# Optimization experiments

Hardware: AMD Instinct MI355X
Metric: run time of the kernel (lower is better)

The kernel has to match this reference:

```python
import jax, jax.numpy as jnp
import numpy as np
from functools import partial

D = 512      # world_state_dim
M = 1000     # memory_size
H = 8        # attention heads
DH = D // H  # head dim
EPS = 1e-5


def _layernorm(x, g, b):
    mu = jnp.mean(x, axis=-1, keepdims=True)
    var = jnp.mean((x - mu) ** 2, axis=-1, keepdims=True)
    return (x - mu) * jax.lax.rsqrt(var + EPS) * g + b


def setup_inputs() -> dict:
    key = jax.random.key(0)
    ks = jax.random.split(key, 24)
    B = 8192
    w = lambda k, shp: (jax.random.normal(k, shp, dtype=jnp.float32) * 0.02)
    inp = {
        "observations": jax.random.normal(ks[0], (B, D), dtype=jnp.float32),
        "ego_motion": jax.random.normal(ks[1], (B, 16), dtype=jnp.float32),
        "world_memory": jax.random.normal(ks[2], (M, D), dtype=jnp.float32) * 0.1,
        # encoder: Linear(D,D) -> ReLU -> LN(D) -> Linear(D,D)
        "enc_w1": w(ks[3], (D, D)), "enc_b1": jnp.zeros((D,), jnp.float32),
        "enc_g": jnp.ones((D,), jnp.float32), "enc_beta": jnp.zeros((D,), jnp.float32),
        "enc_w2": w(ks[4], (D, D)), "enc_b2": jnp.zeros((D,), jnp.float32),
        # multihead attention in/out projections
        "wq": w(ks[5], (D, D)), "bq": jnp.zeros((D,), jnp.float32),
        "wk": w(ks[6], (D, D)), "bk": jnp.zeros((D,), jnp.float32),
        "wv": w(ks[7], (D, D)), "bv": jnp.zeros((D,), jnp.float32),
        "wo": w(ks[8], (D, D)), "bo": jnp.zeros((D,), jnp.float32),
        # transition: Linear(D+16,D) -> ReLU -> LN(D) -> Linear(D,D)
        "tr_w1": w(ks[9], (D, D + 16)), "tr_b1": jnp.zeros((D,), jnp.float32),
        "tr_g": jnp.ones((D,), jnp.float32), "tr_beta": jnp.zeros((D,), jnp.float32),
        "tr_w2": w(ks[10], (D, D)), "tr_b2": jnp.zeros((D,), jnp.float32),
        # quality head: Linear(D,128) -> ReLU -> Linear(128,1) -> Sigmoid
        "q_w1": w(ks[11], (128, D)), "q_b1": jnp.zeros((128,), jnp.float32),
        "q_w2": w(ks[12], (1, 128)), "q_b2": jnp.zeros((1,), jnp.float32),
        # random slots for memory-bank scatter-EMA update (replaces torch.randint)
        "update_indices": jax.random.randint(ks[13], (B,), 0, M, dtype=jnp.int32),
    }
    return inp


def _forward_core(observations, ego_motion, world_memory,
                  enc_w1, enc_b1, enc_g, enc_beta, enc_w2, enc_b2,
                  wq, bq, wk, bk, wv, bv, wo, bo,
                  tr_w1, tr_b1, tr_g, tr_beta, tr_w2, tr_b2,
                  q_w1, q_b1, q_w2, q_b2):
    B = observations.shape[0]
    # world_encoder
    h = jax.nn.relu(observations @ enc_w1.T + enc_b1)
    encoded = _layernorm(h, enc_g, enc_beta) @ enc_w2.T + enc_b2  # [B, D]
    # cross-attention: one query per batch row over shared memory bank
    q = (encoded @ wq.T + bq).reshape(B, H, DH)
    k = (world_memory @ wk.T + bk).reshape(M, H, DH)  # shared across batch
    v = (world_memory @ wv.T + bv).reshape(M, H, DH)
    scores = jnp.einsum("bhd,mhd->bhm", q, k) / jnp.sqrt(jnp.float32(DH))
    attn = jax.nn.softmax(scores, axis=-1)              # [B, H, M]
    ctx = jnp.einsum("bhm,mhd->bhd", attn, v).reshape(B, D)
    memory_states = ctx @ wo.T + bo
    # fuse + transition
    fused = 0.7 * encoded + 0.3 * memory_states
    x = jnp.concatenate([fused, ego_motion], axis=-1)   # [B, D+16]
    h2 = jax.nn.relu(x @ tr_w1.T + tr_b1)
    next_state = _layernorm(h2, tr_g, tr_beta) @ tr_w2.T + tr_b2  # [B, D]
    # quality head
    qh = jax.nn.relu(next_state @ q_w1.T + q_b1)
    quality = jax.nn.sigmoid(qh @ q_w2.T + q_b2)        # [B, 1]
    mem_weights = jnp.mean(attn, axis=1)                # [B, M] avg over heads
    return next_state, quality, mem_weights


def _update_memory_bank(world_memory, next_state, quality, update_indices):
    # Sequential scatter-EMA, faithful to the torch loop (duplicates compound).
    mask = quality[:, 0] > 0.7

    def step(mem, inp):
        idx, st, m = inp
        row = mem[idx]
        new_row = jnp.where(m, 0.9 * row + 0.1 * st, row)
        return mem.at[idx].set(new_row), None

    updated, _ = jax.lax.scan(step, world_memory, (update_indices, next_state, mask))
    return updated


@jax.jit
def reference(observations, ego_motion, world_memory,
              enc_w1, enc_b1, enc_g, enc_beta, enc_w2, enc_b2,
              wq, bq, wk, bk, wv, bv, wo, bo,
              tr_w1, tr_b1, tr_g, tr_beta, tr_w2, tr_b2,
              q_w1, q_b1, q_w2, q_b2, update_indices):
    next_state, quality, mem_weights = _forward_core(
        observations, ego_motion, world_memory,
        enc_w1, enc_b1, enc_g, enc_beta, enc_w2, enc_b2,
        wq, bq, wk, bk, wv, bv, wo, bo,
        tr_w1, tr_b1, tr_g, tr_beta, tr_w2, tr_b2,
        q_w1, q_b1, q_w2, q_b2)
    updated_memory = _update_memory_bank(world_memory, next_state, quality, update_indices)
    return next_state, quality, updated_memory
```

## Files before the change

kernel.cpp:

```cpp
#include <hip/hip_runtime.h>

#define B_ 8192
#define D_ 512
#define M_ 1000
#define H_ 8
#define LOG2E 1.4426950408889634f

typedef unsigned short u16;
typedef __attribute__((ext_vector_type(8))) short bf16x8;
typedef __attribute__((ext_vector_type(4))) float f32x4;

__device__ __forceinline__ float bf2f(u16 u) {
    union { unsigned u; float f; } c; c.u = ((unsigned)u) << 16; return c.f;
}
__device__ __forceinline__ u16 f2bf(float f) {
    union { float f; unsigned u; } c; c.f = f;
    unsigned r = (c.u + 0x7fffu + ((c.u >> 16) & 1u)) >> 16;
    return (u16)r;
}
__device__ __forceinline__ u16 f2bf_fast(float f) {
    union { float f; unsigned u; } c; c.f = f;
    return (u16)((c.u + 0x8000u) >> 16);
}
__device__ __forceinline__ float wave_sum(float v) {
#pragma unroll
    for (int off = 32; off > 0; off >>= 1) v += __shfl_xor(v, off);
    return v;
}

template<bool RELU, bool WF32, bool VTOUT>
__device__ __forceinline__ void gemm_core(
    const u16* __restrict__ A0, const u16* __restrict__ A1,
    const u16* __restrict__ A2, int lda0, int lda1, int lda2,
    const u16* __restrict__ W0, const u16* __restrict__ W1,
    const u16* __restrict__ W2, int ldw0, int ldw1, int ldw2,
    int kb1, int kb2,
    const float* __restrict__ bias, float bscale, float cscale,
    float* __restrict__ Cf, u16* __restrict__ Cb, u16* __restrict__ VT,
    int M, int N, int K, int ldc)
{
    const int m0 = blockIdx.y * 64, n0 = blockIdx.x * 64;
    if (m0 >= M || n0 >= N) return;
    __shared__ u16 As[64 * 64];
    __shared__ u16 Bs[64 * 64];
    const int t = threadIdx.x, w = t >> 6, l = t & 63;
    const int wm = (w >> 1) * 32, wn = (w & 1) * 32;
    const int li = l & 15, quad = l >> 4;

    f32x4 acc[2][2];
#pragma unroll
    for (int i = 0; i < 2; ++i)
#pragma unroll
        for (int j = 0; j < 2; ++j) acc[i][j] = (f32x4){0.f, 0.f, 0.f, 0.f};

    for (int k0 = 0; k0 < K; k0 += 64) {
        const u16* Ab; const u16* Wb; int ldab, ldwb, ko;
        if (k0 < kb1)      { Ab = A0; ldab = lda0; Wb = W0; ldwb = ldw0; ko = k0; }
        else if (k0 < kb2) { Ab = A1; ldab = lda1; Wb = W1; ldwb = ldw1; ko = k0 - kb1; }
        else               { Ab = A2; ldab = lda2; Wb = W2; ldwb = ldw2; ko = k0 - kb2; }
#pragma unroll
        for (int i = 0; i < 2; ++i) {
            const int rl = w * 16 + i * 8 + (l >> 3);
            const int ck = (l & 7) ^ (rl & 7);
            int ga = m0 + rl; ga = ga < M ? ga : M - 1;
            __builtin_amdgcn_global_load_lds(
                (const __attribute__((address_space(1))) void*)(Ab + (size_t)ga * ldab + ko + ck * 8),
                (__attribute__((address_space(3))) void*)(As + (w * 16 + i * 8) * 64),
                16, 0, 0);
        }
#pragma unroll
        for (int i = 0; i < 2; ++i) {
            const int rl = w * 16 + i * 8 + (l >> 3);
            const int ck = (l & 7) ^ (rl & 7);
            int gb = n0 + rl; gb = gb < N ? gb : N - 1;
            __builtin_amdgcn_global_load_lds(
                (const __attribute__((address_space(1))) void*)(Wb + (size_t)gb * ldwb + ko + ck * 8),
                (__attribute__((address_space(3))) void*)(Bs + (w * 16 + i * 8) * 64),
                16, 0, 0);
        }
        __syncthreads();
#pragma unroll
        for (int ks = 0; ks < 2; ++ks) {
            const int ch = ks * 4 + quad;
            bf16x8 af[2], bfr[2];
#pragma unroll
            for (int mt = 0; mt < 2; ++mt) {
                const int r = wm + mt * 16 + li;
                af[mt] = *(const bf16x8*)(As + r * 64 + ((ch ^ (r & 7)) * 8));
            }
#pragma unroll
            for (int nt = 0; nt < 2; ++nt) {
                const int r = wn + nt * 16 + li;
                bfr[nt] = *(const bf16x8*)(Bs + r * 64 + ((ch ^ (r & 7)) * 8));
            }
#pragma unroll
            for (int mt = 0; mt < 2; ++mt)
#pragma unroll
                for (int nt = 0; nt < 2; ++nt)
                    acc[mt][nt] = __builtin_amdgcn_mfma_f32_16x16x32_bf16(
                        af[mt], bfr[nt], acc[mt][nt], 0, 0, 0);
        }
        __syncthreads();
    }

    float bv[2];
#pragma unroll
    for (int nt = 0; nt < 2; ++nt) bv[nt] = bias[n0 + wn + nt * 16 + li] * bscale;
#pragma unroll
    for (int mt = 0; mt < 2; ++mt) {
        const int row0 = m0 + wm + mt * 16 + quad * 4;
#pragma unroll
        for (int nt = 0; nt < 2; ++nt) {
            const int col = n0 + wn + nt * 16 + li;
            if (VTOUT && col >= 512) {
                ushort4 pk;
                u16 pv[4];
#pragma unroll
                for (int r = 0; r < 4; ++r) {
                    float v = acc[mt][nt][r] * cscale + bv[nt];
                    pv[r] = (row0 + r < M_) ? f2bf(v) : (u16)0;
                }
                pk.x = pv[0]; pk.y = pv[1]; pk.z = pv[2]; pk.w = pv[3];
                *(ushort4*)(VT + (size_t)(col - 512) * 1024 + row0) = pk;
            } else {
#pragma unroll
                for (int r = 0; r < 4; ++r) {
                    const int row = row0 + r;
                    if (row >= M) continue;
                    float v = acc[mt][nt][r] * cscale + bv[nt];
                    if (RELU) v = fmaxf(v, 0.f);
                    Cb[(size_t)row * ldc + col] = f2bf(v);
                    if (WF32) Cf[(size_t)row * ldc + col] = v;
                }
            }
        }
    }
}

template<bool RELU, bool WF32>
__launch_bounds__(256)
__global__ void mgemm(const u16* __restrict__ A0, const u16* __restrict__ A1,
                      const u16* __restrict__ A2, int lda0, int lda1, int lda2,
                      const u16* __restrict__ W0, const u16* __restrict__ W1,
                      const u16* __restrict__ W2, int ldw0, int ldw1, int ldw2,
                      int kb1, int kb2,
                      const float* __restrict__ bias, float bscale, float cscale,
                      float* __restrict__ Cf, u16* __restrict__ Cb,
                      int M, int N, int K, int ldc)
{
    gemm_core<RELU, WF32, false>(A0, A1, A2, lda0, lda1, lda2,
                                 W0, W1, W2, ldw0, ldw1, ldw2, kb1, kb2,
                                 bias, bscale, cscale, Cf, Cb, nullptr, M, N, K, ldc);
}

__launch_bounds__(256)
__global__ void foldgemm(const u16* __restrict__ w_q, const u16* __restrict__ w_tr1,
                         const u16* __restrict__ w_e2t, const u16* __restrict__ w_wot,
                         const float* __restrict__ zb,
                         u16* __restrict__ w_qe, u16* __restrict__ w_ae,
                         u16* __restrict__ w_co)
{
    const int z = blockIdx.z;
    if (z == 0)
        gemm_core<false, false, false>(w_q, w_q, w_q, 512, 512, 512,
            w_e2t, w_e2t, w_e2t, 512, 512, 512, 512, 512,
            zb, 0.f, 1.0f, nullptr, w_qe, nullptr, 512, 512, 512, 512);
    else if (z == 1)
        gemm_core<false, false, false>(w_tr1, w_tr1, w_tr1, 576, 576, 576,
            w_e2t, w_e2t, w_e2t, 512, 512, 512, 512, 512,
            zb, 0.f, 0.7f, nullptr, w_ae, nullptr, 512, 512, 512, 512);
    else
        gemm_core<false, false, false>(w_tr1, w_tr1, w_tr1, 576, 576, 576,
            w_wot, w_wot, w_wot, 512, 512, 512, 512, 512,
            zb, 0.f, 0.3f, nullptr, w_co, nullptr, 512, 512, 512, 512);
}

__launch_bounds__(256)
__global__ void qkvgemm(const u16* __restrict__ hn, const u16* __restrict__ w_qe,
                        const float* __restrict__ bqe, u16* __restrict__ qbuf,
                        const u16* __restrict__ wmem_bf, const u16* __restrict__ w_k,
                        const float* __restrict__ bkv, u16* __restrict__ KVbuf,
                        u16* __restrict__ VTb)
{
    if (blockIdx.z == 0)
        gemm_core<false, false, false>(hn, hn, hn, 512, 512, 512,
            w_qe, w_qe, w_qe, 512, 512, 512, 512, 512,
            bqe, 1.f, 1.f, nullptr, qbuf, nullptr, B_, 512, 512, 512);
    else
        gemm_core<false, false, true>(wmem_bf, wmem_bf, wmem_bf, 512, 512, 512,
            w_k, w_k, w_k, 512, 512, 512, 512, 512,
            bkv, 1.f, 1.f, nullptr, KVbuf, VTb, 1024, 1024, 512, 1024);
}

__launch_bounds__(256)
__global__ void attn_kernel(const u16* __restrict__ Q, const u16* __restrict__ KV,
                            const u16* __restrict__ VT, u16* __restrict__ Ob,
                            float* __restrict__ Lb)
{
    __shared__ u16 P[4 * 2048];
    const int t = threadIdx.x, w = t >> 6, l = t & 63;
    const int h = blockIdx.y;
    const int qblk = blockIdx.x & 63, kpart = blockIdx.x >> 6;
    const int q0 = qblk * 128 + w * 32;
    u16* Pw = P + w * 2048;
    const int li = l & 15, quad = l >> 4;

    bf16x8 aq[2][2];
#pragma unroll
    for (int mt = 0; mt < 2; ++mt)
#pragma unroll
        for (int ks = 0; ks < 2; ++ks) {
            const int row = q0 + mt * 16 + li;
            aq[mt][ks] = *(const bf16x8*)(Q + (size_t)row * 512 + h * 64 + ks * 32 + quad * 8);
        }

    bf16x8 ones;
#pragma unroll
    for (int i = 0; i < 8; ++i) ones[i] = (short)0x3F80;

    f32x4 oacc[2][4];
    f32x4 lacc[2];
#pragma unroll
    for (int mt = 0; mt < 2; ++mt) {
        lacc[mt] = (f32x4){0.f, 0.f, 0.f, 0.f};
#pragma unroll
        for (int nt = 0; nt < 4; ++nt) oacc[mt][nt] = (f32x4){0.f, 0.f, 0.f, 0.f};
    }

    const int kbeg = kpart * 512, kend = kbeg + 512;
    for (int kc = kbeg; kc < kend; kc += 64) {
        f32x4 s[2][4];
#pragma unroll
        for (int mt = 0; mt < 2; ++mt)
#pragma unroll
            for (int nt = 0; nt < 4; ++nt) s[mt][nt] = (f32x4){0.f, 0.f, 0.f, 0.f};
#pragma unroll
        for (int ks = 0; ks < 2; ++ks) {
            bf16x8 bk[4];
#pragma unroll
            for (int nt = 0; nt < 4; ++nt) {
                const int key = kc + nt * 16 + li;
                bk[nt] = *(const bf16x8*)(KV + (size_t)key * 1024 + h * 64 + ks * 32 + quad * 8);
            }
#pragma unroll
            for (int mt = 0; mt < 2; ++mt)
#pragma unroll
                for (int nt = 0; nt < 4; ++nt)
                    s[mt][nt] = __builtin_amdgcn_mfma_f32_16x16x32_bf16(
                        aq[mt][ks], bk[nt], s[mt][nt], 0, 0, 0);
        }
        if (kc == 960) {
#pragma unroll
            for (int nt = 0; nt < 4; ++nt) {
                const bool val = (960 + nt * 16 + li) < M_;
#pragma unroll
                for (int mt = 0; mt < 2; ++mt)
#pragma unroll
                    for (int r = 0; r < 4; ++r)
                        if (!val) s[mt][nt][r] = -3.0e38f;
            }
        }
#pragma unroll
        for (int mt = 0; mt < 2; ++mt)
#pragma unroll
            for (int nt = 0; nt < 4; ++nt) {
                const int col = nt * 16 + li;
#pragma unroll
                for (int r = 0; r < 4; ++r) {
                    const float p = exp2f(s[mt][nt][r]);
                    const int rowl = mt * 16 + quad * 4 + r;
                    Pw[rowl * 64 + (((col >> 3) ^ (rowl & 7)) * 8) + (col & 7)] = f2bf_fast(p);
                }
            }
#pragma unroll
        for (int ks = 0; ks < 2; ++ks) {
            const int ch = ks * 4 + quad;
            bf16x8 ap[2];
#pragma unroll
            for (int mt = 0; mt < 2; ++mt) {
                const int rowl = mt * 16 + li;
                ap[mt] = *(const bf16x8*)(Pw + rowl * 64 + ((ch ^ (rowl & 7)) * 8));
            }
#pragma unroll
            for (int mt = 0; mt < 2; ++mt)
                lacc[mt] = __builtin_amdgcn_mfma_f32_16x16x32_bf16(
                    ap[mt], ones, lacc[mt], 0, 0, 0);
#pragma unroll
            for (int nt = 0; nt < 4; ++nt) {
                const bf16x8 bvv = *(const bf16x8*)(VT + ((size_t)(h * 64 + nt * 16 + li)) * 1024 + kc + ks * 32 + quad * 8);
#pragma unroll
                for (int mt = 0; mt < 2; ++mt)
                    oacc[mt][nt] = __builtin_amdgcn_mfma_f32_16x16x32_bf16(
                        ap[mt], bvv, oacc[mt][nt], 0, 0, 0);
            }
        }
    }

    u16* Op = Ob + (size_t)kpart * B_ * 512;
    float* Lp = Lb + (size_t)kpart * B_ * 8;
#pragma unroll
    for (int mt = 0; mt < 2; ++mt)
#pragma unroll
        for (int r = 0; r < 4; ++r) {
            const int row = q0 + mt * 16 + quad * 4 + r;
            if (li == 0) Lp[row * 8 + h] = lacc[mt][r];
#pragma unroll
            for (int nt = 0; nt < 4; ++nt)
                Op[(size_t)row * 512 + h * 64 + nt * 16 + li] = f2bf(oacc[mt][nt][r]);
        }
}

__launch_bounds__(256)
__global__ void attn_combine(const u16* __restrict__ Ob, const float* __restrict__ Lb,
                             u16* __restrict__ ctx)
{
    const int row = blockIdx.x * 4 + (threadIdx.x >> 6);
    const int lane = threadIdx.x & 63;
    const int h = lane >> 3;
    const float inv = 1.0f / (Lb[row * 8 + h] + Lb[(size_t)B_ * 8 + row * 8 + h]);
    const u16* p0 = Ob + (size_t)row * 512 + lane * 8;
    const u16* p1 = p0 + (size_t)B_ * 512;
    uint4 a = *(const uint4*)p0;
    uint4 b = *(const uint4*)p1;
    const unsigned aa[4] = {a.x, a.y, a.z, a.w};
    const unsigned bb[4] = {b.x, b.y, b.z, b.w};
    unsigned o[4];
#pragma unroll
    for (int i = 0; i < 4; ++i) {
        const float lo = (bf2f((u16)(aa[i] & 0xffffu)) + bf2f((u16)(bb[i] & 0xffffu))) * inv;
        const float hi = (bf2f((u16)(aa[i] >> 16)) + bf2f((u16)(bb[i] >> 16))) * inv;
        o[i] = (unsigned)f2bf(lo) | ((unsigned)f2bf(hi) << 16);
    }
    *(uint4*)(ctx + (size_t)row * 512 + lane * 8) = make_uint4(o[0], o[1], o[2], o[3]);
}

__launch_bounds__(256)
__global__ void ln_bf(u16* __restrict__ X, const float* __restrict__ g,
                      const float* __restrict__ be, int rows)
{
    const int row = blockIdx.x * 4 + (threadIdx.x >> 6);
    const int lane = threadIdx.x & 63;
    if (row >= rows) return;
    u16* p = X + (size_t)row * 512 + lane * 8;
    uint4 d = *(const uint4*)p;
    const unsigned dd[4] = {d.x, d.y, d.z, d.w};
    float v[8];
#pragma unroll
    for (int i = 0; i < 4; ++i) {
        v[2 * i]     = bf2f((u16)(dd[i] & 0xffffu));
        v[2 * i + 1] = bf2f((u16)(dd[i] >> 16));
    }
    float s = 0.f;
#pragma unroll
    for (int i = 0; i < 8; ++i) s += v[i];
    s = wave_sum(s);
    const float mu = s * (1.0f / 512.0f);
    float vs = 0.f;
#pragma unroll
    for (int i = 0; i < 8; ++i) { v[i] -= mu; vs += v[i] * v[i]; }
    vs = wave_sum(vs);
    const float r = rsqrtf(vs * (1.0f / 512.0f) + 1e-5f);
    const float* gp = g + lane * 8;
    const float* bp = be + lane * 8;
    unsigned o[4];
#pragma unroll
    for (int i = 0; i < 4; ++i) {
        const u16 lo = f2bf(v[2 * i] * r * gp[2 * i] + bp[2 * i]);
        const u16 hi = f2bf(v[2 * i + 1] * r * gp[2 * i + 1] + bp[2 * i + 1]);
        o[i] = (unsigned)lo | ((unsigned)hi << 16);
    }
    *(uint4*)p = make_uint4(o[0], o[1], o[2], o[3]);
}

__launch_bounds__(256)
__global__ void prep_all(const float* enc_w1, const float* wk_f, const float* wv_f,
                         const float* tr_w2, const float* q_w1, const float* wq,
                         const float* tr_w1, const float* enc_w2, const float* wo,
                         const float* obs, const float* wmem, const float* ego,
                         const float* bk, const float* bvv, const float* bq,
                         const float* enc_b2, const float* trb1, const float* bo,
                         u16* w_enc1, u16* w_k, u16* w_v, u16* w_tr2, u16* w_qh,
                         u16* w_q, u16* w_tr1, u16* w_e2t, u16* w_wot,
                         u16* obs_bf, u16* wmem_bf, u16* ego64,
                         float* bkv, float* bqe, float* btr)
{
    __shared__ float tl[64][65];
    const int seg = blockIdx.y;
    const int t = threadIdx.x;
    const int bx = blockIdx.x;

    if (seg <= 5) {
        const float* s; u16* d; int n; float sc = 1.0f;
        switch (seg) {
            case 0: s = enc_w1; d = w_enc1; n = 262144; break;
            case 1: s = wk_f;   d = w_k;    n = 262144; break;
            case 2: s = wv_f;   d = w_v;    n = 262144; break;
            case 3: s = tr_w2;  d = w_tr2;  n = 262144; break;
            case 4: s = q_w1;   d = w_qh;   n = 65536;  break;
            default: s = wq;    d = w_q;    n = 262144; sc = 0.125f * LOG2E; break;
        }
        const int i0 = (bx * 256 + t) * 4;
        if (i0 + 3 < n) {
            const float4 v = *(const float4*)(s + i0);
            ushort4 o;
            o.x = f2bf(v.x * sc); o.y = f2bf(v.y * sc);
            o.z = f2bf(v.z * sc); o.w = f2bf(v.w * sc);
            *(ushort4*)(d + i0) = o;
        }
    } else if (seg == 6) {
#pragma unroll
        for (int k = 0; k < 4; ++k) {
            const int i = (bx * 256 + t) * 4 + k;
            if (i < 294912) {
                const int r = i / 576, c = i - r * 576;
                w_tr1[i] = (c < 528) ? f2bf(tr_w1[r * 528 + c]) : (u16)0;
            }
        }
    } else if (seg <= 8) {
        if (bx >= 64) return;
        const float* S = (seg == 7) ? enc_w2 : wo;
        u16* D = (seg == 7) ? w_e2t : w_wot;
        const int r0 = (bx >> 3) * 64, c0 = (bx & 7) * 64;
#pragma unroll
        for (int i = 0; i < 16; ++i) {
            const int idx = t + i * 256;
            tl[idx >> 6][idx & 63] = S[(size_t)(r0 + (idx >> 6)) * 512 + c0 + (idx & 63)];
        }
        __syncthreads();
#pragma unroll
        for (int i = 0; i < 16; ++i) {
            const int idx = t + i * 256;
            const int c = idx >> 6, r = idx & 63;
            D[(size_t)(c0 + c) * 512 + r0 + r] = f2bf(tl[r][c]);
        }
    } else if (seg == 9) {
        const int nth = gridDim.x * 256;
        for (int i = bx * 256 + t; i < B_ * 512 / 4; i += nth) {
            const float4 v = ((const float4*)obs)[i];
            ushort4 o;
            o.x = f2bf(v.x); o.y = f2bf(v.y); o.z = f2bf(v.z); o.w = f2bf(v.w);
            ((ushort4*)obs_bf)[i] = o;
        }
    } else if (seg == 10) {
        const int nth = gridDim.x * 256;
        for (int i = bx * 256 + t; i < M_ * 512 / 4; i += nth) {
            const float4 v = ((const float4*)wmem)[i];
            ushort4 o;
            o.x = f2bf(v.x); o.y = f2bf(v.y); o.z = f2bf(v.z); o.w = f2bf(v.w);
            ((ushort4*)wmem_bf)[i] = o;
        }
    } else if (seg == 11) {
        const int nth = gridDim.x * 256;
        for (int i = bx * 256 + t; i < B_ * 64; i += nth) {
            const int b = i >> 6, j = i & 63;
            ego64[(size_t)b * 64 + j] = (j < 16) ? f2bf(ego[b * 16 + j]) : (u16)0;
        }
        const int tid = bx * 256 + t;
        if (tid < 1024) bkv[tid] = (tid < 512) ? bk[tid] : bvv[tid - 512];
    } else {
        if (bx >= 128) return;
        const int i = bx * 4 + (t >> 6);
        const int lane = t & 63;
        float s = 0.f;
        if (seg == 12) {
            const float* wr = wq + (size_t)i * 512 + lane * 8;
#pragma unroll
            for (int j = 0; j < 8; ++j) s += wr[j] * enc_b2[lane * 8 + j];
            s = wave_sum(s);
            if (lane == 0) bqe[i] = 0.125f * LOG2E * (bq[i] + s);
        } else {
            const float* wr = tr_w1 + (size_t)i * 528 + lane * 8;
#pragma unroll
            for (int j = 0; j < 8; ++j)
                s += wr[j] * (0.7f * enc_b2[lane * 8 + j] + 0.3f * bo[lane * 8 + j]);
            s = wave_sum(s);
            if (lane == 0) btr[i] = trb1[i] + s;
        }
    }
}

__global__ void quality_bf(const u16* __restrict__ qh, const float* __restrict__ w2,
                           const float* __restrict__ b2, float* __restrict__ outq,
                           int rows)
{
    const int row = blockIdx.x * 4 + (threadIdx.x >> 6);
    const int lane = threadIdx.x & 63;
    if (row >= rows) return;
    const u16* p = qh + (size_t)row * 128;
    float s = bf2f(p[lane]) * w2[lane] + bf2f(p[64 + lane]) * w2[64 + lane];
    s = wave_sum(s);
    if (lane == 0) outq[row] = 1.0f / (1.0f + expf(-(s + b2[0])));
}

__global__ void compact_kernel(const float* __restrict__ q,
                               int* __restrict__ list, int* __restrict__ cnt)
{
    __shared__ int wtot[16];
    __shared__ int sbase;
    const int t = threadIdx.x, w = t >> 6, lane = t & 63;
    if (t == 0) sbase = 0;
    __syncthreads();
    for (int c = 0; c < B_; c += 1024) {
        const int idx = c + t;
        const bool pred = (q[idx] > 0.7f);
        const unsigned long long bal = __ballot(pred);
        const int prefix = __popcll(bal & ((1ull << lane) - 1ull));
        if (lane == 0) wtot[w] = __popcll(bal);
        __syncthreads();
        int woff = 0;
        for (int i = 0; i < w; ++i) woff += wtot[i];
        if (pred) list[sbase + woff + prefix] = idx;
        __syncthreads();
        if (t == 0) {
            int tot = 0;
            for (int i = 0; i < 16; ++i) tot += wtot[i];
            sbase += tot;
        }
        __syncthreads();
    }
    if (t == 0) *cnt = sbase;
}

__global__ void update_memory_kernel(const float* __restrict__ mem,
                                     const float* __restrict__ ns,
                                     const int* __restrict__ upd,
                                     const int* __restrict__ list,
                                     const int* __restrict__ cnt,
                                     float* __restrict__ outmem)
{
    const int m = blockIdx.x;
    const int t = threadIdx.x;
    const int c4 = t * 4;
    float4 r = *(const float4*)(mem + (size_t)m * D_ + c4);
    const int n = *cnt;
    for (int i = 0; i < n; ++i) {
        const int b = list[i];
        if (upd[b] == m) {
            const float4 s = *(const float4*)(ns + (size_t)b * D_ + c4);
            r.x = 0.9f * r.x + 0.1f * s.x;
            r.y = 0.9f * r.y + 0.1f * s.y;
            r.z = 0.9f * r.z + 0.1f * s.z;
            r.w = 0.9f * r.w + 0.1f * s.w;
        }
    }
    *(float4*)(outmem + (size_t)m * D_ + c4) = r;
}

extern "C" void kernel_launch(void* const* d_in, const int* in_sizes, int n_in,
                              void* d_out, int out_size, void* d_ws, size_t ws_size,
                              hipStream_t stream)
{
    const float* obs    = (const float*)d_in[0];
    const float* ego    = (const float*)d_in[1];
    const float* wmem   = (const float*)d_in[2];
    const float* enc_w1 = (const float*)d_in[3];
    const float* enc_b1 = (const float*)d_in[4];
    const float* enc_g  = (const float*)d_in[5];
    const float* enc_be = (const float*)d_in[6];
    const float* enc_w2 = (const float*)d_in[7];
    const float* enc_b2 = (const float*)d_in[8];
    const float* wq = (const float*)d_in[9];
    const float* bq = (const float*)d_in[10];
    const float* wk_f = (const float*)d_in[11];
    const float* bk = (const float*)d_in[12];
    const float* wv_f = (const float*)d_in[13];
    const float* bvv = (const float*)d_in[14];
    const float* wo = (const float*)d_in[15];
    const float* bo = (const float*)d_in[16];
    const float* tr_w1 = (const float*)d_in[17];
    const float* tr_b1 = (const float*)d_in[18];
    const float* tr_g  = (const float*)d_in[19];
    const float* tr_be = (const float*)d_in[20];
    const float* tr_w2 = (const float*)d_in[21];
    const float* tr_b2 = (const float*)d_in[22];
    const float* q_w1 = (const float*)d_in[23];
    const float* q_b1 = (const float*)d_in[24];
    const float* q_w2 = (const float*)d_in[25];
    const float* q_b2 = (const float*)d_in[26];
    const int*   upd  = (const int*)d_in[27];

    float* out_ns  = (float*)d_out;
    float* out_q   = out_ns + (size_t)B_ * D_;
    float* out_mem = out_q + B_;

    u16* ws = (u16*)d_ws;
    size_t o = 0;
    u16* obs_bf  = ws + o; o += (size_t)B_ * 512;
    u16* wmem_bf = ws + o; o += (size_t)M_ * 512;
    u16* w_enc1  = ws + o; o += 262144;
    u16* w_k     = ws + o; o += 262144;
    u16* w_v     = ws + o; o += 262144;
    u16* w_tr2   = ws + o; o += 262144;
    u16* w_qh    = ws + o; o += 65536;
    u16* w_q     = ws + o; o += 262144;
    u16* w_tr1   = ws + o; o += (size_t)512 * 576;
    u16* w_e2t   = ws + o; o += 262144;
    u16* w_wot   = ws + o; o += 262144;
    u16* w_qe    = ws + o; o += 262144;
    u16* w_ae    = ws + o; o += 262144;
    u16* w_co    = ws + o; o += 262144;
    u16* hbuf    = ws + o; o += (size_t)B_ * 512;
    u16* qbuf    = ws + o; o += (size_t)B_ * 512;
    u16* KVbuf   = ws + o; o += (size_t)1024 * 1024;
    u16* VTb     = ws + o; o += (size_t)512 * 1024;
    u16* ctx     = ws + o; o += (size_t)B_ * 512;
    u16* h2b     = ws + o; o += (size_t)B_ * 512;
    u16* nsbf    = ws + o; o += (size_t)B_ * 512;
    u16* qhb     = ws + o; o += (size_t)B_ * 128;
    u16* ego64   = ws + o; o += (size_t)B_ * 64;
    u16* Obuf    = ws + o; o += (size_t)2 * B_ * 512;
    float* Lbuf  = (float*)(ws + o); o += (size_t)2 * B_ * 8 * 2;
    float* bkv   = (float*)(ws + o); o += 2048;
    float* bqe   = (float*)(ws + o); o += 1024;
    float* btr   = (float*)(ws + o); o += 1024;
    int* list    = (int*)(ws + o);
    int* cnt     = list + B_;

    const dim3 blk(256);

    prep_all<<<dim3(576, 14), blk, 0, stream>>>(
        enc_w1, wk_f, wv_f, tr_w2, q_w1, wq, tr_w1, enc_w2, wo,
        obs, wmem, ego, bk, bvv, bq, enc_b2, tr_b1, bo,
        w_enc1, w_k, w_v, w_tr2, w_qh, w_q, w_tr1, w_e2t, w_wot,
        obs_bf, wmem_bf, ego64, bkv, bqe, btr);

    foldgemm<<<dim3(8, 8, 3), blk, 0, stream>>>(w_q, w_tr1, w_e2t, w_wot, bkv,
                                                w_qe, w_ae, w_co);

    mgemm<true, false><<<dim3(8, 128), blk, 0, stream>>>(
        obs_bf, obs_bf, obs_bf, 512, 512, 512, w_enc1, w_enc1, w_enc1, 512, 512, 512,
        512, 512, enc_b1, 1.f, 1.f, nullptr, hbuf, B_, 512, 512, 512);
    ln_bf<<<dim3(2048), blk, 0, stream>>>(hbuf, enc_g, enc_be, B_);

    qkvgemm<<<dim3(16, 128, 2), blk, 0, stream>>>(
        hbuf, w_qe, bqe, qbuf, wmem_bf, w_k, bkv, KVbuf, VTb);

    attn_kernel<<<dim3(128, 8), blk, 0, stream>>>(qbuf, KVbuf, VTb, Obuf, Lbuf);
    attn_combine<<<dim3(2048), blk, 0, stream>>>(Obuf, Lbuf, ctx);

    mgemm<true, false><<<dim3(8, 128), blk, 0, stream>>>(
        hbuf, ctx, ego64, 512, 512, 64, w_ae, w_co, w_tr1 + 512, 512, 512, 576,
        512, 1024, btr, 1.f, 1.f, nullptr, h2b, B_, 512, 1088, 512);
    ln_bf<<<dim3(2048), blk, 0, stream>>>(h2b, tr_g, tr_be, B_);

    mgemm<false, true><<<dim3(8, 128), blk, 0, stream>>>(
        h2b, h2b, h2b, 512, 512, 512, w_tr2, w_tr2, w_tr2, 512, 512, 512,
        512, 512, tr_b2, 1.f, 1.f, out_ns, nsbf, B_, 512, 512, 512);

    mgemm<true, false><<<dim3(2, 128), blk, 0, stream>>>(
        nsbf, nsbf, nsbf, 512, 512, 512, w_qh, w_qh, w_qh, 512, 512, 512,
        512, 512, q_b1, 1.f, 1.f, nullptr, qhb, B_, 128, 512, 128);
    quality_bf<<<dim3(2048), blk, 0, stream>>>(qhb, q_w2, q_b2, out_q, B_);

    compact_kernel<<<dim3(1), dim3(1024), 0, stream>>>(out_q, list, cnt);
    update_memory_kernel<<<dim3(M_), dim3(128), 0, stream>>>(
        wmem, out_ns, upd, list, cnt, out_mem);
}
```

Before: 305.6 us.

## Double GEMM K-tile to 128 and shrink attention key chunk to 32

The shared GEMM core now stages 128-wide K tiles in LDS with a 16-way XOR swizzle, which halves the number of barrier-separated load/compute rounds per output tile. The attention kernel processes 32 keys per iteration instead of 64 and requests 4 blocks per CU through launch bounds, aiming to cut register pressure and raise occupancy. Because the K tile is now 128, the ego-motion operand is padded to 128 columns and the transition GEMM's K grows to 1152. The extra columns are zero on the activation side, but the weight reads run past the 576-wide rows of tr_w1. The larger tiles also double LDS use per GEMM block.

```diff
diff --git a/kernel.cpp b/kernel.cpp
--- a/kernel.cpp
+++ b/kernel.cpp
@@ -41,8 +41,8 @@
 {
     const int m0 = blockIdx.y * 64, n0 = blockIdx.x * 64;
     if (m0 >= M || n0 >= N) return;
-    __shared__ u16 As[64 * 64];
-    __shared__ u16 Bs[64 * 64];
+    __shared__ u16 As[64 * 128];
+    __shared__ u16 Bs[64 * 128];
     const int t = threadIdx.x, w = t >> 6, l = t & 63;
     const int wm = (w >> 1) * 32, wn = (w & 1) * 32;
     const int li = l & 15, quad = l >> 4;
@@ -53,45 +53,49 @@
 #pragma unroll
         for (int j = 0; j < 2; ++j) acc[i][j] = (f32x4){0.f, 0.f, 0.f, 0.f};
 
-    for (int k0 = 0; k0 < K; k0 += 64) {
+    for (int k0 = 0; k0 < K; k0 += 128) {
         const u16* Ab; const u16* Wb; int ldab, ldwb, ko;
         if (k0 < kb1)      { Ab = A0; ldab = lda0; Wb = W0; ldwb = ldw0; ko = k0; }
         else if (k0 < kb2) { Ab = A1; ldab = lda1; Wb = W1; ldwb = ldw1; ko = k0 - kb1; }
         else               { Ab = A2; ldab = lda2; Wb = W2; ldwb = ldw2; ko = k0 - kb2; }
 #pragma unroll
-        for (int i = 0; i < 2; ++i) {
-            const int rl = w * 16 + i * 8 + (l >> 3);
-            const int ck = (l & 7) ^ (rl & 7);
-            int ga = m0 + rl; ga = ga < M ? ga : M - 1;
+        for (int i = 0; i < 4; ++i) {
+            const int f = i * 256 + t;
+            const int row = f >> 4;
+            const int sl = f & 15;
+            const int ck = sl ^ (row & 15);
+            int ga = m0 + row; ga = ga < M ? ga : M - 1;
             __builtin_amdgcn_global_load_lds(
                 (const __attribute__((address_space(1))) void*)(Ab + (size_t)ga * ldab + ko + ck * 8),
-                (__attribute__((address_space(3))) void*)(As + (w * 16 + i * 8) * 64),
+                (__attribute__((address_space(3))) void*)(As + f * 8),
                 16, 0, 0);
         }
 #pragma unroll
-        for (int i = 0; i < 2; ++i) {
-            const int rl = w * 16 + i * 8 + (l >> 3);
-            const int ck = (l & 7) ^ (rl & 7);
-            int gb = n0 + rl; gb = gb < N ? gb : N - 1;
+        for (int i = 0; i < 4; ++i) {
+            const int f = i * 256 + t;
+            const int row = f >> 4;
+            const int sl = f & 15;
+            const int ck = sl ^ (row & 15);
+            int gb = n0 + row; gb = gb < N ? gb : N - 1;
             __builtin_amdgcn_global_load_lds(
                 (const __attribute__((address_space(1))) void*)(Wb + (size_t)gb * ldwb + ko + ck * 8),
-                (__attribute__((address_space(3))) void*)(Bs + (w * 16 + i * 8) * 64),
+                (__attribute__((address_space(3))) void*)(Bs + f * 8),
                 16, 0, 0);
         }
         __syncthreads();
 #pragma unroll
-        for (int ks = 0; ks < 2; ++ks) {
+        for (int ks = 0; ks < 4; ++ks) {
             const int ch = ks * 4 + quad;
             bf16x8 af[2], bfr[2];
 #pragma unroll
             for (int mt = 0; mt < 2; ++mt) {
                 const int r = wm + mt * 16 + li;
-                af[mt] = *(const bf16x8*)(As + r * 64 + ((ch ^ (r & 7)) * 8));
+                af[mt] = *(const bf16x8*)(As + r * 128 + ((ch ^ (r & 15)) * 8));
             }
 #pragma unroll
             for (int nt = 0; nt < 2; ++nt) {
                 const int r = wn + nt * 16 + li;
-                bfr[nt] = *(const bf16x8*)(Bs + r * 64 + ((ch ^ (r & 7)) * 8));
+                bfr[nt] = *(const bf16x8*)(Bs + r * 128 + ((ch ^ (r & 15)) * 8));
             }
 #pragma unroll
             for (int mt = 0; mt < 2; ++mt)
@@ -192,7 +196,7 @@
             bkv, 1.f, 1.f, nullptr, KVbuf, VTb, 1024, 1024, 512, 1024);
 }
 
-__launch_bounds__(256)
+__launch_bounds__(256, 4)
 __global__ void attn_kernel(const u16* __restrict__ Q, const u16* __restrict__ KV,
                             const u16* __restrict__ VT, u16* __restrict__ Ob,
                             float* __restrict__ Lb)
@@ -228,31 +232,31 @@
     }
 
     const int kbeg = kpart * 512, kend = kbeg + 512;
-    for (int kc = kbeg; kc < kend; kc += 64) {
-        f32x4 s[2][4];
+    for (int kc = kbeg; kc < kend; kc += 32) {
+        f32x4 s[2][2];
 #pragma unroll
         for (int mt = 0; mt < 2; ++mt)
 #pragma unroll
-            for (int nt = 0; nt < 4; ++nt) s[mt][nt] = (f32x4){0.f, 0.f, 0.f, 0.f};
+            for (int nt = 0; nt < 2; ++nt) s[mt][nt] = (f32x4){0.f, 0.f, 0.f, 0.f};
 #pragma unroll
         for (int ks = 0; ks < 2; ++ks) {
-            bf16x8 bk[4];
-#pragma unroll
-            for (int nt = 0; nt < 4; ++nt) {
+            bf16x8 bk[2];
+#pragma unroll
+            for (int nt = 0; nt < 2; ++nt) {
                 const int key = kc + nt * 16 + li;
                 bk[nt] = *(const bf16x8*)(KV + (size_t)key * 1024 + h * 64 + ks * 32 + quad * 8);
             }
 #pragma unroll
             for (int mt = 0; mt < 2; ++mt)
 #pragma unroll
-                for (int nt = 0; nt < 4; ++nt)
+                for (int nt = 0; nt < 2; ++nt)
                     s[mt][nt] = __builtin_amdgcn_mfma_f32_16x16x32_bf16(
                         aq[mt][ks], bk[nt], s[mt][nt], 0, 0, 0);
         }
-        if (kc == 960) {
-#pragma unroll
-            for (int nt = 0; nt < 4; ++nt) {
-                const bool val = (960 + nt * 16 + li) < M_;
+        if (kc == 992) {
+#pragma unroll
+            for (int nt = 0; nt < 2; ++nt) {
+                const bool val = (992 + nt * 16 + li) < M_;
 #pragma unroll
                 for (int mt = 0; mt < 2; ++mt)
 #pragma unroll
@@ -263,36 +267,35 @@
 #pragma unroll
         for (int mt = 0; mt < 2; ++mt)
 #pragma unroll
-            for (int nt = 0; nt < 4; ++nt) {
+            for (int nt = 0; nt < 2; ++nt) {
                 const int col = nt * 16 + li;
+                const int c = col >> 3;
 #pragma unroll
                 for (int r = 0; r < 4; ++r) {
                     const float p = exp2f(s[mt][nt][r]);
-                    const int rowl = mt * 16 + quad * 4 + r;
-                    Pw[rowl * 64 + (((col >> 3) ^ (rowl & 7)) * 8) + (col & 7)] = f2bf_fast(p);
+                    const int row = mt * 16 + quad * 4 + r;
+                    const int slot = (c ^ (row & 3)) | (((row >> 2) & 1) << 2);
+                    Pw[row * 64 + slot * 8 + (col & 7)] = f2bf_fast(p);
                 }
             }
-#pragma unroll
-        for (int ks = 0; ks < 2; ++ks) {
-            const int ch = ks * 4 + quad;
-            bf16x8 ap[2];
-#pragma unroll
-            for (int mt = 0; mt < 2; ++mt) {
-                const int rowl = mt * 16 + li;
-                ap[mt] = *(const bf16x8*)(Pw + rowl * 64 + ((ch ^ (rowl & 7)) * 8));
-            }
+        bf16x8 ap[2];
+#pragma unroll
+        for (int mt = 0; mt < 2; ++mt) {
+            const int row = mt * 16 + li;
+            const int slot = (quad ^ (row & 3)) | (((row >> 2) & 1) << 2);
+            ap[mt] = *(const bf16x8*)(Pw + row * 64 + slot * 8);
+        }
+#pragma unroll
+        for (int mt = 0; mt < 2; ++mt)
+            lacc[mt] = __builtin_amdgcn_mfma_f32_16x16x32_bf16(
+                ap[mt], ones, lacc[mt], 0, 0, 0);
+#pragma unroll
+        for (int nt = 0; nt < 4; ++nt) {
+            const bf16x8 bvv = *(const bf16x8*)(VT + ((size_t)(h * 64 + nt * 16 + li)) * 1024 + kc + quad * 8);
 #pragma unroll
             for (int mt = 0; mt < 2; ++mt)
-                lacc[mt] = __builtin_amdgcn_mfma_f32_16x16x32_bf16(
-                    ap[mt], ones, lacc[mt], 0, 0, 0);
-#pragma unroll
-            for (int nt = 0; nt < 4; ++nt) {
-                const bf16x8 bvv = *(const bf16x8*)(VT + ((size_t)(h * 64 + nt * 16 + li)) * 1024 + kc + ks * 32 + quad * 8);
-#pragma unroll
-                for (int mt = 0; mt < 2; ++mt)
-                    oacc[mt][nt] = __builtin_amdgcn_mfma_f32_16x16x32_bf16(
-                        ap[mt], bvv, oacc[mt][nt], 0, 0, 0);
-            }
+                oacc[mt][nt] = __builtin_amdgcn_mfma_f32_16x16x32_bf16(
+                    ap[mt], bvv, oacc[mt][nt], 0, 0, 0);
         }
     }
 
@@ -381,7 +384,7 @@
                          const float* enc_b2, const float* trb1, const float* bo,
                          u16* w_enc1, u16* w_k, u16* w_v, u16* w_tr2, u16* w_qh,
                          u16* w_q, u16* w_tr1, u16* w_e2t, u16* w_wot,
-                         u16* obs_bf, u16* wmem_bf, u16* ego64,
+                         u16* obs_bf, u16* wmem_bf, u16* ego128,
                          float* bkv, float* bqe, float* btr)
 {
     __shared__ float tl[64][65];
@@ -451,9 +454,9 @@
         }
     } else if (seg == 11) {
         const int nth = gridDim.x * 256;
-        for (int i = bx * 256 + t; i < B_ * 64; i += nth) {
-            const int b = i >> 6, j = i & 63;
-            ego64[(size_t)b * 64 + j] = (j < 16) ? f2bf(ego[b * 16 + j]) : (u16)0;
+        for (int i = bx * 256 + t; i < B_ * 128; i += nth) {
+            const int b = i >> 7, j = i & 127;
+            ego128[(size_t)b * 128 + j] = (j < 16) ? f2bf(ego[b * 16 + j]) : (u16)0;
         }
         const int tid = bx * 256 + t;
         if (tid < 1024) bkv[tid] = (tid < 512) ? bk[tid] : bvv[tid - 512];
@@ -607,7 +610,7 @@
     u16* h2b     = ws + o; o += (size_t)B_ * 512;
     u16* nsbf    = ws + o; o += (size_t)B_ * 512;
     u16* qhb     = ws + o; o += (size_t)B_ * 128;
-    u16* ego64   = ws + o; o += (size_t)B_ * 64;
+    u16* ego128  = ws + o; o += (size_t)B_ * 128;
     u16* Obuf    = ws + o; o += (size_t)2 * B_ * 512;
     float* Lbuf  = (float*)(ws + o); o += (size_t)2 * B_ * 8 * 2;
     float* bkv   = (float*)(ws + o); o += 2048;
@@ -622,7 +625,7 @@
         enc_w1, wk_f, wv_f, tr_w2, q_w1, wq, tr_w1, enc_w2, wo,
         obs, wmem, ego, bk, bvv, bq, enc_b2, tr_b1, bo,
         w_enc1, w_k, w_v, w_tr2, w_qh, w_q, w_tr1, w_e2t, w_wot,
-        obs_bf, wmem_bf, ego64, bkv, bqe, btr);
+        obs_bf, wmem_bf, ego128, bkv, bqe, btr);
 
     foldgemm<<<dim3(8, 8, 3), blk, 0, stream>>>(w_q, w_tr1, w_e2t, w_wot, bkv,
                                                 w_qe, w_ae, w_co);
@@ -639,8 +642,8 @@
     attn_combine<<<dim3(2048), blk, 0, stream>>>(Obuf, Lbuf, ctx);
 
     mgemm<true, false><<<dim3(8, 128), blk, 0, stream>>>(
-        hbuf, ctx, ego64, 512, 512, 64, w_ae, w_co, w_tr1 + 512, 512, 512, 576,
-        512, 1024, btr, 1.f, 1.f, nullptr, h2b, B_, 512, 1088, 512);
+        hbuf, ctx, ego128, 512, 512, 128, w_ae, w_co, w_tr1 + 512, 512, 512, 576,
+        512, 1024, btr, 1.f, 1.f, nullptr, h2b, B_, 512, 1152, 512);
     ln_bf<<<dim3(2048), blk, 0, stream>>>(h2b, tr_g, tr_be, B_);
 
     mgemm<false, true><<<dim3(8, 128), blk, 0, stream>>>(
```

Result: slower. 317.2 us (+3.8%).

## Stage attention K/V tiles into double-buffered LDS via async global loads

Applied to the files above, without the earlier changes.

The attention kernel now copies each 64-key K tile and V^T tile into swizzled, double-buffered shared memory using global_load_lds, prefetching the next tile while computing on the current one. Before this, each of the four waves read K and V directly from global memory, so every tile was fetched four times and load latency was exposed. The change adds a block-wide barrier per iteration and 32KB more LDS, which may reduce occupancy. There is no explicit wait on the async LDS loads beyond __syncthreads, which leaves a correctness risk if the loads have not completed.

```diff
diff --git a/kernel.cpp b/kernel.cpp
--- a/kernel.cpp
+++ b/kernel.cpp
@@ -197,6 +197,8 @@
                             const u16* __restrict__ VT, u16* __restrict__ Ob,
                             float* __restrict__ Lb)
 {
+    __shared__ u16 Ks[2][64 * 64];
+    __shared__ u16 Vs[2][64 * 64];
     __shared__ u16 P[4 * 2048];
     const int t = threadIdx.x, w = t >> 6, l = t & 63;
     const int h = blockIdx.y;
@@ -204,6 +206,7 @@
     const int q0 = qblk * 128 + w * 32;
     u16* Pw = P + w * 2048;
     const int li = l & 15, quad = l >> 4;
+    const int kbeg = kpart * 512;
 
     bf16x8 aq[2][2];
 #pragma unroll
@@ -227,8 +230,37 @@
         for (int nt = 0; nt < 4; ++nt) oacc[mt][nt] = (f32x4){0.f, 0.f, 0.f, 0.f};
     }
 
-    const int kbeg = kpart * 512, kend = kbeg + 512;
-    for (int kc = kbeg; kc < kend; kc += 64) {
+    auto stage = [&](int kc, int buf) {
+#pragma unroll
+        for (int i = 0; i < 2; ++i) {
+            const int f = i * 256 + t;
+            const int r = f >> 3;
+            const int ck = (f & 7) ^ (r & 7);
+            __builtin_amdgcn_global_load_lds(
+                (const __attribute__((address_space(1))) void*)(KV + (size_t)(kc + r) * 1024 + h * 64 + ck * 8),
+                (__attribute__((address_space(3))) void*)(&Ks[buf][f * 8]),
+                16, 0, 0);
+        }
+#pragma unroll
+        for (int i = 0; i < 2; ++i) {
+            const int f = i * 256 + t;
+            const int r = f >> 3;
+            const int ck = (f & 7) ^ (r & 7);
+            __builtin_amdgcn_global_load_lds(
+                (const __attribute__((address_space(1))) void*)(VT + (size_t)(h * 64 + r) * 1024 + kc + ck * 8),
+                (__attribute__((address_space(3))) void*)(&Vs[buf][f * 8]),
+                16, 0, 0);
+        }
+    };
+
+    stage(kbeg, 0);
+    for (int ic = 0; ic < 8; ++ic) {
+        const int kc = kbeg + ic * 64;
+        __syncthreads();
+        if (ic < 7) stage(kc + 64, (ic + 1) & 1);
+        const u16* ksb = &Ks[ic & 1][0];
+        const u16* vsb = &Vs[ic & 1][0];
+
         f32x4 s[2][4];
 #pragma unroll
         for (int mt = 0; mt < 2; ++mt)
@@ -236,11 +268,12 @@
             for (int nt = 0; nt < 4; ++nt) s[mt][nt] = (f32x4){0.f, 0.f, 0.f, 0.f};
 #pragma unroll
         for (int ks = 0; ks < 2; ++ks) {
+            const int ch = ks * 4 + quad;
             bf16x8 bk[4];
 #pragma unroll
             for (int nt = 0; nt < 4; ++nt) {
-                const int key = kc + nt * 16 + li;
-                bk[nt] = *(const bf16x8*)(KV + (size_t)key * 1024 + h * 64 + ks * 32 + quad * 8);
+                const int key = nt * 16 + li;
+                bk[nt] = *(const bf16x8*)(ksb + key * 64 + ((ch ^ (key & 7)) * 8));
             }
 #pragma unroll
             for (int mt = 0; mt < 2; ++mt)
@@ -287,7 +320,8 @@
                     ap[mt], ones, lacc[mt], 0, 0, 0);
 #pragma unroll
             for (int nt = 0; nt < 4; ++nt) {
-                const bf16x8 bvv = *(const bf16x8*)(VT + ((size_t)(h * 64 + nt * 16 + li)) * 1024 + kc + ks * 32 + quad * 8);
+                const int dh = nt * 16 + li;
+                const bf16x8 bvv = *(const bf16x8*)(vsb + dh * 64 + ((ch ^ (dh & 7)) * 8));
 #pragma unroll
                 for (int mt = 0; mt < 2; ++mt)
                     oacc[mt][nt] = __builtin_amdgcn_mfma_f32_16x16x32_bf16(
```

Result: faster. 279.0 us (-8.7%).
